# Kernel optimization log

Measured on AMD Instinct MI355X. Metric: run time of the kernel, lower is better.

The kernel has to match this reference:

```python
import jax, jax.numpy as jnp
import numpy as np

B, T, HID = 2, 2048, 2048
H, KVH, D = 16, 4, 128
N_REP = H // KVH


def _rotate_half(x):
    x1, x2 = jnp.split(x, 2, axis=-1)
    return jnp.concatenate([-x2, x1], axis=-1)


def setup_inputs() -> dict:
    key = jax.random.key(0)
    ks = jax.random.split(key, 8)
    hidden_states = jax.random.normal(ks[0], (B, T, HID), dtype=jnp.float32)
    # RoPE tables: standard theta=10000 frequencies, emb = cat(freqs, freqs)
    inv_freq = 1.0 / (10000.0 ** (np.arange(0, D, 2, dtype=np.float32) / D))
    pos = np.arange(T, dtype=np.float32)
    freqs = np.outer(pos, inv_freq)                      # [T, D/2]
    emb = np.concatenate([freqs, freqs], axis=-1)        # [T, D]
    cos = jnp.broadcast_to(jnp.cos(emb)[None], (B, T, D)).astype(jnp.float32)
    sin = jnp.broadcast_to(jnp.sin(emb)[None], (B, T, D)).astype(jnp.float32)
    # causal additive mask [1,1,T,T]
    neg = jnp.finfo(jnp.float32).min
    causal = jnp.where(jnp.tril(jnp.ones((T, T), dtype=bool)), 0.0, neg)
    attention_mask = causal[None, None].astype(jnp.float32)
    s = 0.02
    Wq = jax.random.normal(ks[1], (H * D, HID), dtype=jnp.float32) * s
    Wk = jax.random.normal(ks[2], (KVH * D, HID), dtype=jnp.float32) * s
    Wv = jax.random.normal(ks[3], (KVH * D, HID), dtype=jnp.float32) * s
    Wo = jax.random.normal(ks[4], (HID, H * D), dtype=jnp.float32) * s
    bq = jnp.zeros((H * D,), dtype=jnp.float32)
    bk = jnp.zeros((KVH * D,), dtype=jnp.float32)
    bv = jnp.zeros((KVH * D,), dtype=jnp.float32)
    return {"hidden_states": hidden_states, "cos": cos, "sin": sin,
            "attention_mask": attention_mask,
            "Wq": Wq, "bq": bq, "Wk": Wk, "bk": bk, "Wv": Wv, "bv": bv, "Wo": Wo}


def reference(hidden_states, cos, sin, attention_mask, Wq, bq, Wk, bk, Wv, bv, Wo):
    bsz, q_len, _ = hidden_states.shape
    q = (jnp.einsum('bth,oh->bto', hidden_states, Wq) + bq).reshape(bsz, q_len, H, D).transpose(0, 2, 1, 3)
    k = (jnp.einsum('bth,oh->bto', hidden_states, Wk) + bk).reshape(bsz, q_len, KVH, D).transpose(0, 2, 1, 3)
    v = (jnp.einsum('bth,oh->bto', hidden_states, Wv) + bv).reshape(bsz, q_len, KVH, D).transpose(0, 2, 1, 3)
    c = cos[:, None, :, :]  # [B,1,T,D]
    s = sin[:, None, :, :]
    q = q * c + _rotate_half(q) * s
    k = k * c + _rotate_half(k) * s
    # repeat KV heads to match Q heads (GQA)
    k = jnp.repeat(k, N_REP, axis=1)  # [B,H,T,D]
    v = jnp.repeat(v, N_REP, axis=1)
    scores = jnp.einsum('bhqd,bhkd->bhqk', q, k) / jnp.sqrt(jnp.float32(D))
    scores = scores + attention_mask
    attn = jax.nn.softmax(scores.astype(jnp.float32), axis=-1).astype(q.dtype)
    out = jnp.einsum('bhqk,bhkd->bhqd', attn, v)          # [B,H,T,D]
    out = out.transpose(0, 2, 1, 3).reshape(bsz, q_len, H * D)
    return jnp.einsum('bto,ho->bth', out, Wo)
```

## Files before the change

### kernel.cpp

```cpp
#include <hip/hip_runtime.h>
#include <hip/hip_bf16.h>
#include <stdint.h>

#define B_ 2
#define T_ 2048
#define HID_ 2048
#define H_ 16
#define KVH_ 4
#define D_ 128

typedef __attribute__((ext_vector_type(8))) short short8;
typedef __attribute__((ext_vector_type(4))) float f32x4;

__device__ __forceinline__ uint16_t f2bf(float x) {
  union { float f; uint32_t u; } c; c.f = x;
  uint32_t r = c.u + 0x7fffu + ((c.u >> 16) & 1u);
  return (uint16_t)(r >> 16);
}
__device__ __forceinline__ float bf2f(uint16_t b) {
  union { uint32_t u; float f; } c; c.u = ((uint32_t)b) << 16;
  return c.f;
}
__device__ __forceinline__ uint16_t hwbf(float x) {
  __hip_bfloat16 h = __float2bfloat16(x);
  return *reinterpret_cast<uint16_t*>(&h);
}

#define XM(r) (((r) & 7) ^ (((r) >> 1) & 4))
#define SC_Q 0.1275523865396698f

__global__ __launch_bounds__(256) void cvt_all(const float* __restrict__ hidden,
                                               const float* __restrict__ Wq,
                                               const float* __restrict__ Wk,
                                               const float* __restrict__ Wv,
                                               const float* __restrict__ Wo,
                                               const float* __restrict__ bq,
                                               const float* __restrict__ bk,
                                               const float* __restrict__ bv,
                                               uint16_t* __restrict__ hidb,
                                               uint16_t* __restrict__ wqkv,
                                               uint16_t* __restrict__ wob,
                                               float* __restrict__ biasq) {
  const int gtid = blockIdx.x * 256 + threadIdx.x;
  const int i = gtid * 4;
  const float* src;
  uint16_t* dst;
  if (i < 8388608)       { src = hidden + i;            dst = hidb + i; }
  else if (i < 12582912) { src = Wq + (i - 8388608);    dst = wqkv + (i - 8388608); }
  else if (i < 13631488) { src = Wk + (i - 12582912);   dst = wqkv + 4194304 + (i - 12582912); }
  else if (i < 14680064) { src = Wv + (i - 13631488);   dst = wqkv + 5242880 + (i - 13631488); }
  else                   { src = Wo + (i - 14680064);   dst = wob + (i - 14680064); }
  const float4 v = *reinterpret_cast<const float4*>(src);
  union { uint16_t s[4]; uint2 u; } pk;
  pk.s[0] = f2bf(v.x); pk.s[1] = f2bf(v.y); pk.s[2] = f2bf(v.z); pk.s[3] = f2bf(v.w);
  *reinterpret_cast<uint2*>(dst) = pk.u;
  if (gtid < 3072)
    biasq[gtid] = (gtid < 2048) ? bq[gtid] : (gtid < 2560) ? bk[gtid - 2048] : bv[gtid - 2560];
}

#define BM 128
#define BN 128
#define BK 64

__global__ __launch_bounds__(512, 4) void gemm_qkv(const uint16_t* __restrict__ A,
                                                   const uint16_t* __restrict__ Bt,
                                                   const float* __restrict__ bias,
                                                   const float* __restrict__ cosp,
                                                   const float* __restrict__ sinp,
                                                   uint16_t* __restrict__ Qo,
                                                   uint16_t* __restrict__ Ko,
                                                   uint16_t* __restrict__ VtG) {
  __shared__ __align__(16) uint16_t Al[2][BM * BK];
  __shared__ __align__(16) uint16_t Bl[2][BN * BK];
  const int K = 2048;
  const int tid = threadIdx.x;
  const int w = tid >> 6;
  const int lane = tid & 63;
  const int wr = w >> 1, wc = w & 1;
  const int lm = lane & 15, lg = lane >> 4;

  const int GX = gridDim.x;
  const int nwg = GX * gridDim.y;
  int bid = blockIdx.y * GX + blockIdx.x;
  bid = (bid & 7) * (nwg >> 3) + (bid >> 3);
  const int bm = (bid / GX) * BM;
  const int bn = (bid % GX) * BN;

  const int colb[4] = {wc * 32, wc * 32 + 16, wc * 32 + 64, wc * 32 + 80};

  f32x4 acc[2][4];
  const f32x4 z4 = {0.f, 0.f, 0.f, 0.f};
#pragma unroll
  for (int i = 0; i < 2; ++i)
#pragma unroll
    for (int j = 0; j < 4; ++j) acc[i][j] = z4;

  const int nt = K >> 6;

  auto stage = [&](int b, int t) {
    const int k0 = t * BK;
#pragma unroll
    for (int it = 0; it < 2; ++it) {
      const int chunk = it * 512 + tid;
      const int r = chunk >> 3, c8 = chunk & 7;
      const int csw = (c8 ^ XM(r)) * 8;
      const uint16_t* gA = A + (size_t)(bm + r) * K + k0 + csw;
      const uint16_t* gB = Bt + (size_t)(bn + r) * K + k0 + csw;
      __builtin_amdgcn_global_load_lds((const __attribute__((address_space(1))) unsigned int*)gA,
                                       (__attribute__((address_space(3))) unsigned int*)(&Al[b][0] + chunk * 8),
                                       16, 0, 0);
      __builtin_amdgcn_global_load_lds((const __attribute__((address_space(1))) unsigned int*)gB,
                                       (__attribute__((address_space(3))) unsigned int*)(&Bl[b][0] + chunk * 8),
                                       16, 0, 0);
    }
  };

  stage(0, 0);
  __syncthreads();

  int cur = 0;
  for (int t = 0; t < nt; ++t) {
    if (t + 1 < nt) stage(cur ^ 1, t + 1);
#pragma unroll
    for (int kk = 0; kk < 2; ++kk) {
      short8 af[2], bfr[4];
#pragma unroll
      for (int mi = 0; mi < 2; ++mi) {
        const int r = wr * 32 + mi * 16 + lm;
        af[mi] = *reinterpret_cast<const short8*>(&Al[cur][r * BK + (((kk * 4 + lg) ^ XM(r)) * 8)]);
      }
#pragma unroll
      for (int ni = 0; ni < 4; ++ni) {
        const int r = colb[ni] + lm;
        bfr[ni] = *reinterpret_cast<const short8*>(&Bl[cur][r * BK + (((kk * 4 + lg) ^ XM(r)) * 8)]);
      }
#pragma unroll
      for (int mi = 0; mi < 2; ++mi)
#pragma unroll
        for (int ni = 0; ni < 4; ++ni)
          acc[mi][ni] = __builtin_amdgcn_mfma_f32_16x16x32_bf16(af[mi], bfr[ni], acc[mi][ni], 0, 0, 0);
    }
    __syncthreads();
    cur ^= 1;
  }

  float bb[4];
#pragma unroll
  for (int ni = 0; ni < 4; ++ni) bb[ni] = bias[bn + colb[ni] + lm];

  if (bn < 2560) {
    const bool isQ = (bn < 2048);
    const int head = isQ ? (bn >> 7) : ((bn - 2048) >> 7);
    const int nh = isQ ? H_ : KVH_;
    uint16_t* dst = isQ ? Qo : Ko;
    const float sc = isQ ? SC_Q : 1.0f;
#pragma unroll
    for (int mi = 0; mi < 2; ++mi) {
#pragma unroll
      for (int r = 0; r < 4; ++r) {
        const int row = bm + wr * 32 + mi * 16 + lg * 4 + r;
        const int b = row >> 11, tt = row & 2047;
        const float* cr = cosp + ((size_t)b * T_ + tt) * D_;
        const float* sr = sinp + ((size_t)b * T_ + tt) * D_;
        uint16_t* drow = dst + (((size_t)(b * nh + head)) * T_ + tt) * D_;
#pragma unroll
        for (int ni = 0; ni < 4; ++ni) {
          const int d = colb[ni] + lm;
          const float xv = acc[mi][ni][r] + bb[ni];
          const float pv = acc[mi][ni ^ 2][r] + bb[ni ^ 2];
          const float sgn = (ni < 2) ? -1.f : 1.f;
          drow[d] = f2bf((xv * cr[d] + sgn * pv * sr[d]) * sc);
        }
      }
    }
  } else {
    const int kvh = (bn - 2560) >> 7;
#pragma unroll
    for (int mi = 0; mi < 2; ++mi) {
      const int row0 = bm + wr * 32 + mi * 16 + lg * 4;
      const int b = row0 >> 11, t0 = row0 & 2047;
#pragma unroll
      for (int ni = 0; ni < 4; ++ni) {
        const int d = colb[ni] + lm;
        union { uint16_t s[4]; uint2 u; } pk;
#pragma unroll
        for (int r = 0; r < 4; ++r) pk.s[r] = f2bf(acc[mi][ni][r] + bb[ni]);
        *reinterpret_cast<uint2*>(VtG + ((size_t)(b * KVH_ + kvh) * D_ + d) * T_ + t0) = pk.u;
      }
    }
  }
}

__global__ __launch_bounds__(512, 4) void gemm_bt(const uint16_t* __restrict__ A,
                                                  const uint16_t* __restrict__ Bt,
                                                  float* __restrict__ Cv,
                                                  int M, int N, int K) {
  __shared__ __align__(16) uint16_t Al[2][BM * BK];
  __shared__ __align__(16) uint16_t Bl[2][BN * BK];
  const int tid = threadIdx.x;
  const int w = tid >> 6;
  const int lane = tid & 63;
  const int wr = w >> 1, wc = w & 1;
  const int lm = lane & 15, lg = lane >> 4;

  const int GX = gridDim.x;
  const int nwg = GX * gridDim.y;
  int bid = blockIdx.y * GX + blockIdx.x;
  bid = (bid & 7) * (nwg >> 3) + (bid >> 3);
  const int bm = (bid / GX) * BM;
  const int bn = (bid % GX) * BN;

  f32x4 acc[2][4];
  const f32x4 z4 = {0.f, 0.f, 0.f, 0.f};
#pragma unroll
  for (int i = 0; i < 2; ++i)
#pragma unroll
    for (int j = 0; j < 4; ++j) acc[i][j] = z4;

  const int nt = K >> 6;

  auto stage = [&](int b, int t) {
    const int k0 = t * BK;
#pragma unroll
    for (int it = 0; it < 2; ++it) {
      const int chunk = it * 512 + tid;
      const int r = chunk >> 3, c8 = chunk & 7;
      const int csw = (c8 ^ XM(r)) * 8;
      const uint16_t* gA = A + (size_t)(bm + r) * K + k0 + csw;
      const uint16_t* gB = Bt + (size_t)(bn + r) * K + k0 + csw;
      __builtin_amdgcn_global_load_lds((const __attribute__((address_space(1))) unsigned int*)gA,
                                       (__attribute__((address_space(3))) unsigned int*)(&Al[b][0] + chunk * 8),
                                       16, 0, 0);
      __builtin_amdgcn_global_load_lds((const __attribute__((address_space(1))) unsigned int*)gB,
                                       (__attribute__((address_space(3))) unsigned int*)(&Bl[b][0] + chunk * 8),
                                       16, 0, 0);
    }
  };

  stage(0, 0);
  __syncthreads();

  int cur = 0;
  for (int t = 0; t < nt; ++t) {
    if (t + 1 < nt) stage(cur ^ 1, t + 1);
#pragma unroll
    for (int kk = 0; kk < 2; ++kk) {
      short8 af[2], bfr[4];
#pragma unroll
      for (int mi = 0; mi < 2; ++mi) {
        const int r = wr * 32 + mi * 16 + lm;
        af[mi] = *reinterpret_cast<const short8*>(&Al[cur][r * BK + (((kk * 4 + lg) ^ XM(r)) * 8)]);
      }
#pragma unroll
      for (int ni = 0; ni < 4; ++ni) {
        const int r = wc * 64 + ni * 16 + lm;
        bfr[ni] = *reinterpret_cast<const short8*>(&Bl[cur][r * BK + (((kk * 4 + lg) ^ XM(r)) * 8)]);
      }
#pragma unroll
      for (int mi = 0; mi < 2; ++mi)
#pragma unroll
        for (int ni = 0; ni < 4; ++ni)
          acc[mi][ni] = __builtin_amdgcn_mfma_f32_16x16x32_bf16(af[mi], bfr[ni], acc[mi][ni], 0, 0, 0);
    }
    __syncthreads();
    cur ^= 1;
  }

#pragma unroll
  for (int mi = 0; mi < 2; ++mi) {
#pragma unroll
    for (int ni = 0; ni < 4; ++ni) {
      const int col = bn + wc * 64 + ni * 16 + lm;
#pragma unroll
      for (int r = 0; r < 4; ++r) {
        const int row = bm + wr * 32 + mi * 16 + lg * 4 + r;
        Cv[(size_t)row * N + col] = acc[mi][ni][r];
      }
    }
  }
}

#define KVBLK 64

__global__ __launch_bounds__(256, 2) void attn_fwd(const uint16_t* __restrict__ Qb,
                                                   const uint16_t* __restrict__ Kb,
                                                   const uint16_t* __restrict__ VtG,
                                                   uint16_t* __restrict__ Ab) {
  __shared__ __align__(16) uint16_t Kl[2][KVBLK * D_];
  __shared__ __align__(16) uint16_t Vtl[2][D_ * KVBLK];
  __shared__ __align__(16) uint16_t Pl[4 * 16 * 64];
  const int tid = threadIdx.x;
  const int w = tid >> 6, lane = tid & 63;
  const int lm = lane & 15, lg = lane >> 4;
  const int bh = blockIdx.y;
  const int b = bh >> 4, h = bh & 15;
  const int kvh = h >> 2;
  const int qtA = (blockIdx.x + bh) & 15;
  const int qtB = 31 - qtA;
  const int nA = qtA + 1;
  const int ntot = 33;

  const uint16_t* Kbase = Kb + ((size_t)(b * KVH_ + kvh)) * T_ * D_;
  const uint16_t* Vtbase = VtG + ((size_t)(b * KVH_ + kvh)) * D_ * T_;
  uint16_t* Pw = Pl + w * 16 * 64;
  const f32x4 z4 = {0.f, 0.f, 0.f, 0.f};

  short8 vone;
#pragma unroll
  for (int j = 0; j < 8; ++j) vone[j] = (short)0x3F80;

  f32x4 o[8];
  f32x4 osum;
  float mrow[4];
  short8 qf[4];

  auto loadQ = [&](int qt) {
    const uint16_t* Qw = Qb + (((size_t)(b * H_ + h)) * T_ + qt * 64 + w * 16) * D_;
#pragma unroll
    for (int kk = 0; kk < 4; ++kk)
      qf[kk] = *reinterpret_cast<const short8*>(Qw + (size_t)lm * D_ + kk * 32 + lg * 8);
  };
  auto resetAcc = [&]() {
#pragma unroll
    for (int f = 0; f < 8; ++f) o[f] = z4;
    osum = z4;
#pragma unroll
    for (int r = 0; r < 4; ++r) mrow[r] = -1e30f;
  };
  auto flush = [&](int qt) {
    const int wr0 = qt * 64 + w * 16;
    float rcp[4];
#pragma unroll
    for (int r = 0; r < 4; ++r) rcp[r] = 1.0f / osum[r];
#pragma unroll
    for (int f = 0; f < 8; ++f) {
      const int col = h * D_ + f * 16 + lm;
#pragma unroll
      for (int r = 0; r < 4; ++r) {
        const int trow = wr0 + lg * 4 + r;
        Ab[((size_t)(b * T_ + trow)) * (H_ * D_) + col] = f2bf(o[f][r] * rcp[r]);
      }
    }
  };
  auto stage = [&](int buf, int kv0) {
#pragma unroll
    for (int it = 0; it < 4; ++it) {
      const int chunk = it * 256 + tid;
      {
        const int r = chunk >> 4, c16 = chunk & 15;
        const uint16_t* g = Kbase + (size_t)(kv0 + r) * D_ + ((c16 ^ XM(r)) * 8);
        __builtin_amdgcn_global_load_lds((const __attribute__((address_space(1))) unsigned int*)g,
                                         (__attribute__((address_space(3))) unsigned int*)(&Kl[buf][0] + (it * 256 + w * 64) * 8),
                                         16, 0, 0);
      }
      {
        const int dd = chunk >> 3, c8 = chunk & 7;
        const uint16_t* g = Vtbase + (size_t)dd * T_ + kv0 + ((c8 ^ XM(dd)) * 8);
        __builtin_amdgcn_global_load_lds((const __attribute__((address_space(1))) unsigned int*)g,
                                         (__attribute__((address_space(3))) unsigned int*)(&Vtl[buf][0] + (it * 256 + w * 64) * 8),
                                         16, 0, 0);
      }
    }
  };

  loadQ(qtA);
  resetAcc();
  stage(0, 0);
  __syncthreads();

  int cur = 0;
  for (int g = 0; g < ntot; ++g) {
    const bool inA = g < nA;
    const int t = inA ? g : g - nA;
    const int qt = inA ? qtA : qtB;
    const int kv0 = t * KVBLK;
    const int wrow0 = qt * 64 + w * 16;

    if (g + 1 < ntot) {
      const int gn = g + 1;
      const int kvn = (gn < nA ? gn : gn - nA) * KVBLK;
      stage(cur ^ 1, kvn);
    }

    f32x4 s[4];
#pragma unroll
    for (int nf = 0; nf < 4; ++nf) s[nf] = z4;
#pragma unroll
    for (int nf = 0; nf < 4; ++nf)
#pragma unroll
      for (int kk = 0; kk < 4; ++kk) {
        const int row = nf * 16 + lm;
        const short8 kf = *reinterpret_cast<const short8*>(&Kl[cur][row * D_ + (((kk * 4 + lg) ^ XM(row)) * 8)]);
        s[nf] = __builtin_amdgcn_mfma_f32_16x16x32_bf16(qf[kk], kf, s[nf], 0, 0, 0);
      }

    if (kv0 + KVBLK - 1 > wrow0) {
#pragma unroll
      for (int nf = 0; nf < 4; ++nf) {
        const int colg = kv0 + nf * 16 + lm;
#pragma unroll
        for (int r = 0; r < 4; ++r) {
          const int rowg = wrow0 + lg * 4 + r;
          if (colg > rowg) s[nf][r] = -1e30f;
        }
      }
    }

    float tmax[4];
#pragma unroll
    for (int r = 0; r < 4; ++r)
      tmax[r] = fmaxf(fmaxf(s[0][r], s[1][r]), fmaxf(s[2][r], s[3][r]));
    bool grow = false;
#pragma unroll
    for (int r = 0; r < 4; ++r) grow = grow || (tmax[r] > mrow[r] + 8.f);
    if (__any((int)grow)) {
#pragma unroll
      for (int r = 0; r < 4; ++r) {
        float v = tmax[r];
        v = fmaxf(v, __shfl_xor(v, 1));
        v = fmaxf(v, __shfl_xor(v, 2));
        v = fmaxf(v, __shfl_xor(v, 4));
        v = fmaxf(v, __shfl_xor(v, 8));
        const float nm = fmaxf(mrow[r], v);
        const float al = exp2f(mrow[r] - nm);
        mrow[r] = nm;
        osum[r] *= al;
#pragma unroll
        for (int f = 0; f < 8; ++f) o[f][r] *= al;
      }
    }
#pragma unroll
    for (int nf = 0; nf < 4; ++nf)
#pragma unroll
      for (int r = 0; r < 4; ++r) {
        const float p = exp2f(s[nf][r] - mrow[r]);
        const int prow = lg * 4 + r;
        const int pchunk = (nf * 2 + (lm >> 3)) ^ XM(prow);
        Pw[prow * 64 + pchunk * 8 + (lm & 7)] = hwbf(p);
      }
    asm volatile("s_waitcnt lgkmcnt(0)" ::: "memory");
    short8 pf[2];
#pragma unroll
    for (int ks = 0; ks < 2; ++ks)
      pf[ks] = *reinterpret_cast<const short8*>(Pw + lm * 64 + (((ks * 4 + lg) ^ XM(lm)) * 8));
#pragma unroll
    for (int ks = 0; ks < 2; ++ks)
      osum = __builtin_amdgcn_mfma_f32_16x16x32_bf16(pf[ks], vone, osum, 0, 0, 0);
#pragma unroll
    for (int f = 0; f < 8; ++f)
#pragma unroll
      for (int ks = 0; ks < 2; ++ks) {
        const int dd = f * 16 + lm;
        const short8 vf = *reinterpret_cast<const short8*>(&Vtl[cur][dd * KVBLK + (((ks * 4 + lg) ^ XM(dd)) * 8)]);
        o[f] = __builtin_amdgcn_mfma_f32_16x16x32_bf16(pf[ks], vf, o[f], 0, 0, 0);
      }

    __syncthreads();
    cur ^= 1;

    if (g == nA - 1) {
      flush(qtA);
      loadQ(qtB);
      resetAcc();
    }
  }
  flush(qtB);
}

extern "C" void kernel_launch(void* const* d_in, const int* in_sizes, int n_in,
                              void* d_out, int out_size, void* d_ws, size_t ws_size,
                              hipStream_t stream) {
  const float* hidden = (const float*)d_in[0];
  const float* cosp   = (const float*)d_in[1];
  const float* sinp   = (const float*)d_in[2];
  const float* Wq = (const float*)d_in[4];
  const float* bq = (const float*)d_in[5];
  const float* Wk = (const float*)d_in[6];
  const float* bk = (const float*)d_in[7];
  const float* Wv = (const float*)d_in[8];
  const float* bv = (const float*)d_in[9];
  const float* Wo = (const float*)d_in[10];

  char* ws = (char*)d_ws;
  uint16_t* hidb   = (uint16_t*)(ws);
  uint16_t* wqkv   = (uint16_t*)(ws + 16777216);
  uint16_t* wob    = (uint16_t*)(ws + 29360128);
  float*    biasq  = (float*)   (ws + 37748736);
  uint16_t* Qb     = (uint16_t*)(ws + 62926848);
  uint16_t* Kb     = (uint16_t*)(ws + 79704064);
  uint16_t* VtG    = (uint16_t*)(ws + 83898368);
  uint16_t* Ab     = (uint16_t*)(ws + 88092672);

  cvt_all<<<18432, 256, 0, stream>>>(hidden, Wq, Wk, Wv, Wo, bq, bk, bv,
                                     hidb, wqkv, wob, biasq);
  gemm_qkv<<<dim3(24, 32), 512, 0, stream>>>(hidb, wqkv, biasq, cosp, sinp, Qb, Kb, VtG);
  attn_fwd<<<dim3(16, 32), 256, 0, stream>>>(Qb, Kb, VtG, Ab);
  gemm_bt<<<dim3(16, 32), 512, 0, stream>>>(Ab, wob, (float*)d_out, 4096, 2048, 2048);
}
```

Before: 207.8 us.

## Enlarge QKV GEMM tiles to 256x256 and remap blocks per XCD

The fused QKV+RoPE GEMM moves from 128x128 to 256x256 tiles. Each wave now computes 128x64 with 8x4 MFMA accumulators, which raises arithmetic intensity and LDS reuse, and the epilogue index math changes to match. Both GEMMs replace the simple XCD swizzle with an explicit mapping so that each XCD works on a contiguous sub-grid of tiles, aiming for better L2 locality. The cost is a grid of only 192 workgroups for the QKV GEMM (possibly under one wave of CUs), more registers, lower occupancy and 128KB of LDS per block.

```diff
diff --git a/kernel.cpp b/kernel.cpp
--- a/kernel.cpp
+++ b/kernel.cpp
@@ -58,11 +58,11 @@
     biasq[gtid] = (gtid < 2048) ? bq[gtid] : (gtid < 2560) ? bk[gtid - 2048] : bv[gtid - 2560];
 }
 
-#define BM 128
-#define BN 128
+#define QBM 256
+#define QBN 256
 #define BK 64
 
-__global__ __launch_bounds__(512, 4) void gemm_qkv(const uint16_t* __restrict__ A,
+__global__ __launch_bounds__(512, 2) void gemm_qkv(const uint16_t* __restrict__ A,
                                                    const uint16_t* __restrict__ Bt,
                                                    const float* __restrict__ bias,
                                                    const float* __restrict__ cosp,
@@ -70,28 +70,28 @@
                                                    uint16_t* __restrict__ Qo,
                                                    uint16_t* __restrict__ Ko,
                                                    uint16_t* __restrict__ VtG) {
-  __shared__ __align__(16) uint16_t Al[2][BM * BK];
-  __shared__ __align__(16) uint16_t Bl[2][BN * BK];
+  __shared__ __align__(16) uint16_t Al[2][QBM * BK];
+  __shared__ __align__(16) uint16_t Bl[2][QBN * BK];
   const int K = 2048;
   const int tid = threadIdx.x;
   const int w = tid >> 6;
   const int lane = tid & 63;
-  const int wr = w >> 1, wc = w & 1;
+  const int wr = w >> 2, wc = w & 3;
   const int lm = lane & 15, lg = lane >> 4;
 
-  const int GX = gridDim.x;
-  const int nwg = GX * gridDim.y;
-  int bid = blockIdx.y * GX + blockIdx.x;
-  bid = (bid & 7) * (nwg >> 3) + (bid >> 3);
-  const int bm = (bid / GX) * BM;
-  const int bn = (bid % GX) * BN;
-
-  const int colb[4] = {wc * 32, wc * 32 + 16, wc * 32 + 64, wc * 32 + 80};
-
-  f32x4 acc[2][4];
+  const int orig = blockIdx.y * gridDim.x + blockIdx.x;
+  const int xcd = orig & 7;
+  const int cc = orig >> 3;
+  const int bm = ((xcd & 3) * 4 + (cc & 3)) * QBM;
+  const int bn = ((xcd >> 2) * 6 + (cc >> 2)) * QBN;
+
+  const int cb0 = (wc >> 1) * 128 + (wc & 1) * 32;
+  const int colb[4] = {cb0, cb0 + 16, cb0 + 64, cb0 + 80};
+
+  f32x4 acc[8][4];
   const f32x4 z4 = {0.f, 0.f, 0.f, 0.f};
 #pragma unroll
-  for (int i = 0; i < 2; ++i)
+  for (int i = 0; i < 8; ++i)
 #pragma unroll
     for (int j = 0; j < 4; ++j) acc[i][j] = z4;
 
@@ -100,7 +100,7 @@
   auto stage = [&](int b, int t) {
     const int k0 = t * BK;
 #pragma unroll
-    for (int it = 0; it < 2; ++it) {
+    for (int it = 0; it < 4; ++it) {
       const int chunk = it * 512 + tid;
       const int r = chunk >> 3, c8 = chunk & 7;
       const int csw = (c8 ^ XM(r)) * 8;
@@ -123,22 +123,20 @@
     if (t + 1 < nt) stage(cur ^ 1, t + 1);
 #pragma unroll
     for (int kk = 0; kk < 2; ++kk) {
-      short8 af[2], bfr[4];
-#pragma unroll
-      for (int mi = 0; mi < 2; ++mi) {
-        const int r = wr * 32 + mi * 16 + lm;
-        af[mi] = *reinterpret_cast<const short8*>(&Al[cur][r * BK + (((kk * 4 + lg) ^ XM(r)) * 8)]);
-      }
+      short8 bfr[4];
 #pragma unroll
       for (int ni = 0; ni < 4; ++ni) {
-        const int r = colb[ni] + lm;
-        bfr[ni] = *reinterpret_cast<const short8*>(&Bl[cur][r * BK + (((kk * 4 + lg) ^ XM(r)) * 8)]);
-      }
-#pragma unroll
-      for (int mi = 0; mi < 2; ++mi)
+        const int rb = colb[ni] + lm;
+        bfr[ni] = *reinterpret_cast<const short8*>(&Bl[cur][rb * BK + (((kk * 4 + lg) ^ XM(rb)) * 8)]);
+      }
+#pragma unroll
+      for (int mi = 0; mi < 8; ++mi) {
+        const int r = wr * 128 + mi * 16 + lm;
+        const short8 af = *reinterpret_cast<const short8*>(&Al[cur][r * BK + (((kk * 4 + lg) ^ XM(r)) * 8)]);
 #pragma unroll
         for (int ni = 0; ni < 4; ++ni)
-          acc[mi][ni] = __builtin_amdgcn_mfma_f32_16x16x32_bf16(af[mi], bfr[ni], acc[mi][ni], 0, 0, 0);
+          acc[mi][ni] = __builtin_amdgcn_mfma_f32_16x16x32_bf16(af, bfr[ni], acc[mi][ni], 0, 0, 0);
+      }
     }
     __syncthreads();
     cur ^= 1;
@@ -150,22 +148,22 @@
 
   if (bn < 2560) {
     const bool isQ = (bn < 2048);
-    const int head = isQ ? (bn >> 7) : ((bn - 2048) >> 7);
+    const int head0 = (isQ ? (bn >> 7) : ((bn - 2048) >> 7)) + (wc >> 1);
     const int nh = isQ ? H_ : KVH_;
     uint16_t* dst = isQ ? Qo : Ko;
     const float sc = isQ ? SC_Q : 1.0f;
 #pragma unroll
-    for (int mi = 0; mi < 2; ++mi) {
+    for (int mi = 0; mi < 8; ++mi) {
 #pragma unroll
       for (int r = 0; r < 4; ++r) {
-        const int row = bm + wr * 32 + mi * 16 + lg * 4 + r;
+        const int row = bm + wr * 128 + mi * 16 + lg * 4 + r;
         const int b = row >> 11, tt = row & 2047;
         const float* cr = cosp + ((size_t)b * T_ + tt) * D_;
         const float* sr = sinp + ((size_t)b * T_ + tt) * D_;
-        uint16_t* drow = dst + (((size_t)(b * nh + head)) * T_ + tt) * D_;
+        uint16_t* drow = dst + (((size_t)(b * nh + head0)) * T_ + tt) * D_;
 #pragma unroll
         for (int ni = 0; ni < 4; ++ni) {
-          const int d = colb[ni] + lm;
+          const int d = (wc & 1) * 32 + (ni & 1) * 16 + (ni >> 1) * 64 + lm;
           const float xv = acc[mi][ni][r] + bb[ni];
           const float pv = acc[mi][ni ^ 2][r] + bb[ni ^ 2];
           const float sgn = (ni < 2) ? -1.f : 1.f;
@@ -174,14 +172,14 @@
       }
     }
   } else {
-    const int kvh = (bn - 2560) >> 7;
-#pragma unroll
-    for (int mi = 0; mi < 2; ++mi) {
-      const int row0 = bm + wr * 32 + mi * 16 + lg * 4;
+    const int kvh = ((bn - 2560) >> 7) + (wc >> 1);
+#pragma unroll
+    for (int mi = 0; mi < 8; ++mi) {
+      const int row0 = bm + wr * 128 + mi * 16 + lg * 4;
       const int b = row0 >> 11, t0 = row0 & 2047;
 #pragma unroll
       for (int ni = 0; ni < 4; ++ni) {
-        const int d = colb[ni] + lm;
+        const int d = (wc & 1) * 32 + (ni & 1) * 16 + (ni >> 1) * 64 + lm;
         union { uint16_t s[4]; uint2 u; } pk;
 #pragma unroll
         for (int r = 0; r < 4; ++r) pk.s[r] = f2bf(acc[mi][ni][r] + bb[ni]);
@@ -190,6 +188,9 @@
     }
   }
 }
+
+#define BM 128
+#define BN 128
 
 __global__ __launch_bounds__(512, 4) void gemm_bt(const uint16_t* __restrict__ A,
                                                   const uint16_t* __restrict__ Bt,
@@ -204,11 +205,11 @@
   const int lm = lane & 15, lg = lane >> 4;
 
   const int GX = gridDim.x;
-  const int nwg = GX * gridDim.y;
-  int bid = blockIdx.y * GX + blockIdx.x;
-  bid = (bid & 7) * (nwg >> 3) + (bid >> 3);
-  const int bm = (bid / GX) * BM;
-  const int bn = (bid % GX) * BN;
+  const int orig = blockIdx.y * GX + blockIdx.x;
+  const int xcd = orig & 7;
+  const int cc = orig >> 3;
+  const int bm = ((xcd >> 1) * 8 + (cc & 7)) * BM;
+  const int bn = ((xcd & 1) * (GX >> 1) + (cc >> 3)) * BN;
 
   f32x4 acc[2][4];
   const f32x4 z4 = {0.f, 0.f, 0.f, 0.f};
@@ -493,7 +494,7 @@
 
   cvt_all<<<18432, 256, 0, stream>>>(hidden, Wq, Wk, Wv, Wo, bq, bk, bv,
                                      hidb, wqkv, wob, biasq);
-  gemm_qkv<<<dim3(24, 32), 512, 0, stream>>>(hidb, wqkv, biasq, cosp, sinp, Qb, Kb, VtG);
+  gemm_qkv<<<dim3(12, 16), 512, 0, stream>>>(hidb, wqkv, biasq, cosp, sinp, Qb, Kb, VtG);
   attn_fwd<<<dim3(16, 32), 256, 0, stream>>>(Qb, Kb, VtG, Ab);
   gemm_bt<<<dim3(16, 32), 512, 0, stream>>>(Ab, wob, (float*)d_out, 4096, 2048, 2048);
 }
```

New measurement: 200.3 us. 1.04x faster.

## Deepen GEMM pipelines to four LDS stages and remap blocks for XCD locality

Applied to the files above, without the earlier changes.

Both GEMM kernels move from double buffering to a four-stage LDS ring, prefetching three K-tiles ahead and replacing __syncthreads with explicit vmcnt waits plus s_barrier. This is meant to hide more global-load latency. Block-to-tile mapping is rewritten so each XCD covers a contiguous 8x(N/2) tile region, and the attention grid is flattened so blocks sharing a KV head land on the same XCD, both aimed at better L2 reuse. The cost is that LDS per block doubles to 128KB, so occupancy drops and launch bounds fall to 2 blocks, and the hard-coded vmcnt counts depend on exactly four loads per stage.

```diff
diff --git a/kernel.cpp b/kernel.cpp
--- a/kernel.cpp
+++ b/kernel.cpp
@@ -62,7 +62,7 @@
 #define BN 128
 #define BK 64
 
-__global__ __launch_bounds__(512, 4) void gemm_qkv(const uint16_t* __restrict__ A,
+__global__ __launch_bounds__(512, 2) void gemm_qkv(const uint16_t* __restrict__ A,
                                                    const uint16_t* __restrict__ Bt,
                                                    const float* __restrict__ bias,
                                                    const float* __restrict__ cosp,
@@ -70,8 +70,8 @@
                                                    uint16_t* __restrict__ Qo,
                                                    uint16_t* __restrict__ Ko,
                                                    uint16_t* __restrict__ VtG) {
-  __shared__ __align__(16) uint16_t Al[2][BM * BK];
-  __shared__ __align__(16) uint16_t Bl[2][BN * BK];
+  __shared__ __align__(16) uint16_t Al[4][BM * BK];
+  __shared__ __align__(16) uint16_t Bl[4][BN * BK];
   const int K = 2048;
   const int tid = threadIdx.x;
   const int w = tid >> 6;
@@ -79,12 +79,11 @@
   const int wr = w >> 1, wc = w & 1;
   const int lm = lane & 15, lg = lane >> 4;
 
-  const int GX = gridDim.x;
-  const int nwg = GX * gridDim.y;
-  int bid = blockIdx.y * GX + blockIdx.x;
-  bid = (bid & 7) * (nwg >> 3) + (bid >> 3);
-  const int bm = (bid / GX) * BM;
-  const int bn = (bid % GX) * BN;
+  const int orig = blockIdx.y * gridDim.x + blockIdx.x;
+  const int xcd = orig & 7;
+  const int cc = orig >> 3;
+  const int bm = ((xcd >> 1) * 8 + (cc & 7)) * BM;
+  const int bn = ((xcd & 1) * 12 + (cc >> 3)) * BN;
 
   const int colb[4] = {wc * 32, wc * 32 + 16, wc * 32 + 64, wc * 32 + 80};
 
@@ -116,23 +115,26 @@
   };
 
   stage(0, 0);
-  __syncthreads();
-
-  int cur = 0;
+  stage(1, 1);
+  stage(2, 2);
+  asm volatile("s_waitcnt vmcnt(8)" ::: "memory");
+  __builtin_amdgcn_s_barrier();
+
+  int bc = 0;
   for (int t = 0; t < nt; ++t) {
-    if (t + 1 < nt) stage(cur ^ 1, t + 1);
+    if (t + 3 < nt) stage((bc + 3) & 3, t + 3);
 #pragma unroll
     for (int kk = 0; kk < 2; ++kk) {
       short8 af[2], bfr[4];
 #pragma unroll
       for (int mi = 0; mi < 2; ++mi) {
         const int r = wr * 32 + mi * 16 + lm;
-        af[mi] = *reinterpret_cast<const short8*>(&Al[cur][r * BK + (((kk * 4 + lg) ^ XM(r)) * 8)]);
+        af[mi] = *reinterpret_cast<const short8*>(&Al[bc][r * BK + (((kk * 4 + lg) ^ XM(r)) * 8)]);
       }
 #pragma unroll
       for (int ni = 0; ni < 4; ++ni) {
         const int r = colb[ni] + lm;
-        bfr[ni] = *reinterpret_cast<const short8*>(&Bl[cur][r * BK + (((kk * 4 + lg) ^ XM(r)) * 8)]);
+        bfr[ni] = *reinterpret_cast<const short8*>(&Bl[bc][r * BK + (((kk * 4 + lg) ^ XM(r)) * 8)]);
       }
 #pragma unroll
       for (int mi = 0; mi < 2; ++mi)
@@ -140,8 +142,11 @@
         for (int ni = 0; ni < 4; ++ni)
           acc[mi][ni] = __builtin_amdgcn_mfma_f32_16x16x32_bf16(af[mi], bfr[ni], acc[mi][ni], 0, 0, 0);
     }
-    __syncthreads();
-    cur ^= 1;
+    if (t + 3 < nt)      asm volatile("s_waitcnt vmcnt(8)" ::: "memory");
+    else if (t + 2 < nt) asm volatile("s_waitcnt vmcnt(4)" ::: "memory");
+    else if (t + 1 < nt) asm volatile("s_waitcnt vmcnt(0)" ::: "memory");
+    __builtin_amdgcn_s_barrier();
+    bc = (bc + 1) & 3;
   }
 
   float bb[4];
@@ -191,12 +196,12 @@
   }
 }
 
-__global__ __launch_bounds__(512, 4) void gemm_bt(const uint16_t* __restrict__ A,
+__global__ __launch_bounds__(512, 2) void gemm_bt(const uint16_t* __restrict__ A,
                                                   const uint16_t* __restrict__ Bt,
                                                   float* __restrict__ Cv,
                                                   int M, int N, int K) {
-  __shared__ __align__(16) uint16_t Al[2][BM * BK];
-  __shared__ __align__(16) uint16_t Bl[2][BN * BK];
+  __shared__ __align__(16) uint16_t Al[4][BM * BK];
+  __shared__ __align__(16) uint16_t Bl[4][BN * BK];
   const int tid = threadIdx.x;
   const int w = tid >> 6;
   const int lane = tid & 63;
@@ -204,11 +209,11 @@
   const int lm = lane & 15, lg = lane >> 4;
 
   const int GX = gridDim.x;
-  const int nwg = GX * gridDim.y;
-  int bid = blockIdx.y * GX + blockIdx.x;
-  bid = (bid & 7) * (nwg >> 3) + (bid >> 3);
-  const int bm = (bid / GX) * BM;
-  const int bn = (bid % GX) * BN;
+  const int orig = blockIdx.y * GX + blockIdx.x;
+  const int xcd = orig & 7;
+  const int cc = orig >> 3;
+  const int bm = ((xcd >> 1) * 8 + (cc & 7)) * BM;
+  const int bn = ((xcd & 1) * (GX >> 1) + (cc >> 3)) * BN;
 
   f32x4 acc[2][4];
   const f32x4 z4 = {0.f, 0.f, 0.f, 0.f};
@@ -238,23 +243,26 @@
   };
 
   stage(0, 0);
-  __syncthreads();
-
-  int cur = 0;
+  stage(1, 1);
+  stage(2, 2);
+  asm volatile("s_waitcnt vmcnt(8)" ::: "memory");
+  __builtin_amdgcn_s_barrier();
+
+  int bc = 0;
   for (int t = 0; t < nt; ++t) {
-    if (t + 1 < nt) stage(cur ^ 1, t + 1);
+    if (t + 3 < nt) stage((bc + 3) & 3, t + 3);
 #pragma unroll
     for (int kk = 0; kk < 2; ++kk) {
       short8 af[2], bfr[4];
 #pragma unroll
       for (int mi = 0; mi < 2; ++mi) {
         const int r = wr * 32 + mi * 16 + lm;
-        af[mi] = *reinterpret_cast<const short8*>(&Al[cur][r * BK + (((kk * 4 + lg) ^ XM(r)) * 8)]);
+        af[mi] = *reinterpret_cast<const short8*>(&Al[bc][r * BK + (((kk * 4 + lg) ^ XM(r)) * 8)]);
       }
 #pragma unroll
       for (int ni = 0; ni < 4; ++ni) {
         const int r = wc * 64 + ni * 16 + lm;
-        bfr[ni] = *reinterpret_cast<const short8*>(&Bl[cur][r * BK + (((kk * 4 + lg) ^ XM(r)) * 8)]);
+        bfr[ni] = *reinterpret_cast<const short8*>(&Bl[bc][r * BK + (((kk * 4 + lg) ^ XM(r)) * 8)]);
       }
 #pragma unroll
       for (int mi = 0; mi < 2; ++mi)
@@ -262,8 +270,11 @@
         for (int ni = 0; ni < 4; ++ni)
           acc[mi][ni] = __builtin_amdgcn_mfma_f32_16x16x32_bf16(af[mi], bfr[ni], acc[mi][ni], 0, 0, 0);
     }
-    __syncthreads();
-    cur ^= 1;
+    if (t + 3 < nt)      asm volatile("s_waitcnt vmcnt(8)" ::: "memory");
+    else if (t + 2 < nt) asm volatile("s_waitcnt vmcnt(4)" ::: "memory");
+    else if (t + 1 < nt) asm volatile("s_waitcnt vmcnt(0)" ::: "memory");
+    __builtin_amdgcn_s_barrier();
+    bc = (bc + 1) & 3;
   }
 
 #pragma unroll
@@ -292,10 +303,13 @@
   const int tid = threadIdx.x;
   const int w = tid >> 6, lane = tid & 63;
   const int lm = lane & 15, lg = lane >> 4;
-  const int bh = blockIdx.y;
-  const int b = bh >> 4, h = bh & 15;
-  const int kvh = h >> 2;
-  const int qtA = (blockIdx.x + bh) & 15;
+  const int grp = blockIdx.x & 7;
+  const int i0 = blockIdx.x >> 3;
+  const int b = grp >> 2, kvh = grp & 3;
+  const int h = kvh * 4 + (i0 >> 4);
+  const int bh = b * 16 + h;
+  const int x = i0 & 15;
+  const int qtA = (x + bh) & 15;
   const int qtB = 31 - qtA;
   const int nA = qtA + 1;
   const int ntot = 33;
@@ -494,6 +508,6 @@
   cvt_all<<<18432, 256, 0, stream>>>(hidden, Wq, Wk, Wv, Wo, bq, bk, bv,
                                      hidb, wqkv, wob, biasq);
   gemm_qkv<<<dim3(24, 32), 512, 0, stream>>>(hidb, wqkv, biasq, cosp, sinp, Qb, Kb, VtG);
-  attn_fwd<<<dim3(16, 32), 256, 0, stream>>>(Qb, Kb, VtG, Ab);
+  attn_fwd<<<512, 256, 0, stream>>>(Qb, Kb, VtG, Ab);
   gemm_bt<<<dim3(16, 32), 512, 0, stream>>>(Ab, wob, (float*)d_out, 4096, 2048, 2048);
 }
```

Result: slower. 260.9 us (+25.6%).
